# Optimization experiments

Hardware: AMD Instinct MI355X
Metric: run time of the kernel (lower is better)

The kernel has to match this reference:

```python
import jax, jax.numpy as jnp
import numpy as np

N, NFEAT, NHID, NCLASS, HEADS, NLAYERS, E = 10000, 128, 64, 16, 4, 4, 160000
DT = 0.01
EPS = 1e-05


def _rmsnorm(x):
    rms = jnp.sqrt(jnp.mean(x * x, axis=-1, keepdims=True) + EPS)
    return x / rms


def setup_inputs() -> dict:
    key = jax.random.key(0)
    ks = jax.random.split(key, 16)
    s = lambda fi, fo: 1.0 / np.sqrt(fi)
    def lin(k, fi, fo):
        k1, k2 = jax.random.split(k)
        lim = 1.0 / np.sqrt(fi)
        return (jax.random.uniform(k1, (fi, fo), jnp.float32, -lim, lim),
                jax.random.uniform(k2, (fo,), jnp.float32, -lim, lim))
    x = jax.random.normal(ks[0], (N, NFEAT), jnp.float32)
    edge_index = jax.random.randint(ks[1], (2, E), 0, N, dtype=jnp.int64)
    enc_w, enc_b = lin(ks[2], NFEAT, NHID)
    dec_w, dec_b = lin(ks[3], NHID, NCLASS)
    lo_w, lo_b = lin(ks[4], NHID * HEADS, NHID)
    dpl_w, dpl_b = lin(ks[5], NHID, NHID * HEADS)
    dpr_w, dpr_b = lin(ks[6], NHID, NHID * HEADS)
    lin_w, lin_b = lin(ks[7], NHID, NHID * HEADS)
    att = jax.random.normal(ks[8], (HEADS, NHID), jnp.float32) * (1.0 / np.sqrt(NHID))
    return dict(x=x, enc_w=enc_w, enc_b=enc_b, dec_w=dec_w, dec_b=dec_b,
                lo_w=lo_w, lo_b=lo_b, dpl_w=dpl_w, dpl_b=dpl_b,
                dpr_w=dpr_w, dpr_b=dpr_b, lin_w=lin_w, lin_b=lin_b,
                att=att, edge_index=edge_index)


def reference(x, enc_w, enc_b, dec_w, dec_b, lo_w, lo_b, dpl_w, dpl_b,
              dpr_w, dpr_b, lin_w, lin_b, att, edge_index):
    row, col = edge_index[0], edge_index[1]  # src, dst

    # dynamics constants (learnable_dyn_params=False)
    omega = jax.nn.softplus(jnp.float32(1.0))
    zeta = jax.nn.softplus(jnp.float32(1.0))
    Ks = jax.nn.softplus(jnp.float32(1.0))
    omega_sq = omega * omega

    Y = jax.nn.relu(x @ enc_w + enc_b)              # [N, nhid]
    X = Y

    # fixed GATv2 attention projections from Y_0
    xl = (Y @ dpl_w + dpl_b).reshape(N, HEADS, NHID)  # [N,H,C]
    xr = (Y @ dpr_w + dpr_b).reshape(N, HEADS, NHID)

    # symmetric GCN normalization on edges
    deg = jax.ops.segment_sum(jnp.ones((E,), jnp.float32), col, num_segments=N)
    dis = jnp.where(deg > 0, deg ** -0.5, 0.0)
    norm = dis[row] * dis[col]                       # [E]

    # edge attention logits are fixed across layers (depend only on Y_0)
    e_feat = jax.nn.leaky_relu(xl[row] + xr[col], 0.2)      # [E,H,C]
    score = jnp.einsum('ehc,hc->eh', e_feat, att)           # [E,H]
    smax = jax.ops.segment_max(score, col, num_segments=N)  # [N,H]
    a = jnp.exp(score - smax[col])
    ssum = jax.ops.segment_sum(a, col, num_segments=N)      # [N,H]
    alpha = a / jnp.where(ssum[col] > 0, ssum[col], 1.0)    # [E,H]
    w_edge = alpha * norm[:, None]                          # [E,H]

    for _ in range(NLAYERS):
        v = (Y @ lin_w + lin_b).reshape(N, HEADS, NHID)     # value projection
        msg = v[row] * w_edge[:, :, None]                   # [E,H,C]
        coupling = jax.ops.segment_sum(msg, col, num_segments=N).reshape(N, HEADS * NHID)
        coupling_Y = coupling @ lo_w + lo_b                 # [N, nhid]
        Y = Y + DT * (-2.0 * zeta * omega * Y - omega_sq * X + Ks * coupling_Y)
        X = X + DT * Y
        X = _rmsnorm(X)
        Y = _rmsnorm(Y)

    return X @ dec_w + dec_b                                # [N, nclass]
```

## Files before the change

### kernel.cpp

```cpp
#include <hip/hip_runtime.h>
#include <math.h>

#define NFEAT 128
#define HC    256
#define NCLS  16
#define DT_F  0.01f
#define EPS_F 1e-5f

__device__ __forceinline__ unsigned char f2f8(float f) {
  int v = __builtin_amdgcn_cvt_pk_fp8_f32(f, f, 0, false);
  return (unsigned char)(v & 0xff);
}
__device__ __forceinline__ float f82f(unsigned int b) {
  return __builtin_amdgcn_cvt_f32_fp8((int)b, 0);
}
__device__ __forceinline__ float f82f_sel0(unsigned int w) { return __builtin_amdgcn_cvt_f32_fp8((int)w, 0); }
__device__ __forceinline__ float f82f_sel1(unsigned int w) { return __builtin_amdgcn_cvt_f32_fp8((int)w, 1); }
__device__ __forceinline__ float f82f_sel2(unsigned int w) { return __builtin_amdgcn_cvt_f32_fp8((int)w, 2); }
__device__ __forceinline__ float f82f_sel3(unsigned int w) { return __builtin_amdgcn_cvt_f32_fp8((int)w, 3); }

__device__ __forceinline__ float edge_logit(unsigned int w, float4 r4, float4 at4) {
  float vx = f82f_sel0(w) + r4.x, vy = f82f_sel1(w) + r4.y;
  float vz = f82f_sel2(w) + r4.z, vw = f82f_sel3(w) + r4.w;
  vx = fmaxf(vx, 0.2f * vx); vy = fmaxf(vy, 0.2f * vy);
  vz = fmaxf(vz, 0.2f * vz); vw = fmaxf(vw, 0.2f * vw);
  float t = vx * at4.x;
  t = fmaf(vy, at4.y, t); t = fmaf(vz, at4.z, t); t = fmaf(vw, at4.w, t);
  return t;
}

__global__ __launch_bounds__(256) void enc_kernel(
    const float* __restrict__ x, const float* __restrict__ w,
    const float* __restrict__ b, float* __restrict__ Y, float* __restrict__ X,
    unsigned char* __restrict__ Ybf, int* __restrict__ deg, int n) {
  __shared__ float ws[NFEAT * 64];
  const int gtid = blockIdx.x * 256 + threadIdx.x, GSZ = gridDim.x * 256;
  for (int t = gtid; t < n; t += GSZ) deg[t] = 0;
  for (int t = threadIdx.x; t < NFEAT * 64; t += blockDim.x) ws[t] = w[t];
  __syncthreads();
  const int wave = threadIdx.x >> 6, lane = threadIdx.x & 63;
  for (int i = blockIdx.x * 4 + wave; i < n; i += gridDim.x * 4) {
    const float* xr = x + (size_t)i * NFEAT;
    float acc = b[lane];
#pragma unroll 8
    for (int k = 0; k < NFEAT; ++k) acc = fmaf(xr[k], ws[k * 64 + lane], acc);
    acc = fmaxf(acc, 0.f);
    const size_t idx = (size_t)i * 64 + lane;
    Y[idx] = acc; X[idx] = acc; Ybf[idx] = f2f8(acc);
  }
}

__global__ __launch_bounds__(256) void proj_kernel(
    const float* __restrict__ Y,
    const float* __restrict__ wl, const float* __restrict__ bl,
    const float* __restrict__ wr, const float* __restrict__ br,
    const int* __restrict__ col, const float* __restrict__ lin_w,
    const float* __restrict__ lin_b, const float* __restrict__ lo_w,
    unsigned char* __restrict__ xlb, float* __restrict__ xr,
    float* __restrict__ Wext, float* __restrict__ bb, int* __restrict__ deg,
    int n, int E) {
  const int half = gridDim.x >> 1;
  const bool doR = (int)blockIdx.x < half;
  const int bid = doR ? blockIdx.x : blockIdx.x - half;
  const float* __restrict__ W = doR ? wr : wl;
  const float* __restrict__ B = doR ? br : bl;
  float wreg[64];
  const int t = threadIdx.x;
#pragma unroll
  for (int k = 0; k < 64; ++k) wreg[k] = W[k * HC + t];
  const float bias = B[t];
  for (int i0 = bid * 4; i0 < n; i0 += half * 4) {
    const float* ap = Y + (size_t)i0 * 64;
    float a0 = bias, a1 = bias, a2 = bias, a3 = bias;
#pragma unroll
    for (int k = 0; k < 64; ++k) {
      const float w = wreg[k];
      a0 = fmaf(ap[k], w, a0);
      a1 = fmaf(ap[64 + k], w, a1);
      a2 = fmaf(ap[128 + k], w, a2);
      a3 = fmaf(ap[192 + k], w, a3);
    }
    if (doR) {
      if (i0 + 0 < n) xr[(size_t)(i0 + 0) * HC + t] = a0;
      if (i0 + 1 < n) xr[(size_t)(i0 + 1) * HC + t] = a1;
      if (i0 + 2 < n) xr[(size_t)(i0 + 2) * HC + t] = a2;
      if (i0 + 3 < n) xr[(size_t)(i0 + 3) * HC + t] = a3;
    } else {
      if (i0 + 0 < n) xlb[(size_t)(i0 + 0) * HC + t] = f2f8(a0);
      if (i0 + 1 < n) xlb[(size_t)(i0 + 1) * HC + t] = f2f8(a1);
      if (i0 + 2 < n) xlb[(size_t)(i0 + 2) * HC + t] = f2f8(a2);
      if (i0 + 3 < n) xlb[(size_t)(i0 + 3) * HC + t] = f2f8(a3);
    }
  }
  const int gtid = blockIdx.x * 256 + t, GSZ = gridDim.x * 256;
  for (int e = gtid; e < E; e += GSZ) atomicAdd(&deg[col[e]], 1);
  for (int f = gtid; f < 260 * 64; f += GSZ) {
    const int b2 = f >> 6, j = f & 63;
    float a = 0.f;
    if (b2 < 256) {
      const int k = b2 >> 2, h = b2 & 3;
#pragma unroll 8
      for (int c = 0; c < 64; ++c)
        a = fmaf(lin_w[k * HC + h * 64 + c], lo_w[(size_t)(h * 64 + c) * 64 + j], a);
      Wext[b2 * 64 + j] = a;
    } else {
      const int h = b2 - 256;
#pragma unroll 8
      for (int c = 0; c < 64; ++c)
        a = fmaf(lin_b[h * 64 + c], lo_w[(size_t)(h * 64 + c) * 64 + j], a);
      bb[h * 64 + j] = a;
    }
  }
}

__global__ __launch_bounds__(1024) void scan_kernel(
    const int* __restrict__ deg, int* __restrict__ offsets, int* __restrict__ cursor,
    float* __restrict__ dis, int n) {
  __shared__ int part[1024];
  const int t = threadIdx.x;
  const int chunk = (n + 1023) / 1024;
  const int start = t * chunk;
  const int end = min(start + chunk, n);
  int s = 0;
  for (int i = start; i < end; ++i) s += deg[i];
  part[t] = s;
  __syncthreads();
  for (int off = 1; off < 1024; off <<= 1) {
    int v = (t >= off) ? part[t - off] : 0;
    __syncthreads();
    part[t] += v;
    __syncthreads();
  }
  int run = (t == 0) ? 0 : part[t - 1];
  for (int i = start; i < end; ++i) {
    offsets[i] = run;
    cursor[i] = run;
    const int d = deg[i];
    dis[i] = (d > 0) ? rsqrtf((float)d) : 0.f;
    run += d;
  }
}

__global__ __launch_bounds__(256) void scatter_kernel(
    const int* __restrict__ row, const int* __restrict__ col,
    int* __restrict__ cursor, int* __restrict__ srow, int E) {
  int e = blockIdx.x * blockDim.x + threadIdx.x;
  if (e >= E) return;
  int pos = atomicAdd(&cursor[col[e]], 1);
  srow[pos] = row[e];
}

__global__ __launch_bounds__(256, 8) void score_layer1(
    const int* __restrict__ offs, const int* __restrict__ deg,
    const int* __restrict__ srow,
    const unsigned char* __restrict__ xlb, const float* __restrict__ xr,
    const float* __restrict__ att, const float* __restrict__ dis,
    const float* __restrict__ bb, const float* __restrict__ lo_b,
    const float* __restrict__ Wext, const unsigned char* __restrict__ ybf_in,
    const float* __restrict__ Yin, float* __restrict__ Yout,
    unsigned char* __restrict__ ybf_out, float* __restrict__ X,
    float4* __restrict__ sw, float4* __restrict__ invq, float* __restrict__ fb,
    int n, float c_decay, float c_x, float c_k) {
  const int tid = threadIdx.x, wave = tid >> 6, lane = tid & 63;
  __shared__ float aggl[4][HC];
  __shared__ float partl[4][4][64];
  const float4 at4 = ((const float4*)att)[lane];
  const unsigned int* xlb4 = (const unsigned int*)xlb;
  const float4* xr4 = (const float4*)xr;
  const int i = blockIdx.x * 4 + wave;
  float g0 = 0.f, g1 = 0.f, g2 = 0.f, g3 = 0.f;
  float fbv = 0.f;
  if (i < n) {
    const int s = offs[i], e = s + deg[i];
    if (s >= e) {
      if (lane == 0) invq[i] = make_float4(0.f, 0.f, 0.f, 0.f);
      fbv = lo_b[lane];
      fb[(size_t)i * 64 + lane] = fbv;
    } else {
      const float4 r4 = xr4[(size_t)i * 64 + lane];
      const float dd = dis[i];
      float ssum = 0.f, wsum = 0.f;
      int p = s;
      int n0 = 0, n1 = 0, n2 = 0, n3 = 0;
      if (p + 3 < e) { n0 = srow[p]; n1 = srow[p + 1]; n2 = srow[p + 2]; n3 = srow[p + 3]; }
      while (p + 3 < e) {
        const int q0 = n0, q1 = n1, q2 = n2, q3 = n3;
        const int pn = p + 4;
        if (pn + 3 < e) { n0 = srow[pn]; n1 = srow[pn + 1]; n2 = srow[pn + 2]; n3 = srow[pn + 3]; }
        const unsigned int u0 = xlb4[(size_t)q0 * 64 + lane];
        const unsigned int u1 = xlb4[(size_t)q1 * 64 + lane];
        const unsigned int u2 = xlb4[(size_t)q2 * 64 + lane];
        const unsigned int u3 = xlb4[(size_t)q3 * 64 + lane];
        const float di0 = dis[q0], di1 = dis[q1], di2 = dis[q2], di3 = dis[q3];
        const float ya = f82f(ybf_in[(size_t)q0 * 64 + lane]);
        const float yb = f82f(ybf_in[(size_t)q1 * 64 + lane]);
        const float yc = f82f(ybf_in[(size_t)q2 * 64 + lane]);
        const float yd = f82f(ybf_in[(size_t)q3 * 64 + lane]);
        float t0 = edge_logit(u0, r4, at4);
        float t1 = edge_logit(u1, r4, at4);
        float t2 = edge_logit(u2, r4, at4);
        float t3 = edge_logit(u3, r4, at4);
#pragma unroll
        for (int m = 1; m < 16; m <<= 1) {
          t0 += __shfl_xor(t0, m);
          t1 += __shfl_xor(t1, m);
          t2 += __shfl_xor(t2, m);
          t3 += __shfl_xor(t3, m);
        }
        const float a0 = __expf(t0), a1 = __expf(t1), a2 = __expf(t2), a3 = __expf(t3);
        ssum += (a0 + a1) + (a2 + a3);
        const float sv0 = a0 * di0, sv1 = a1 * di1, sv2 = a2 * di2, sv3 = a3 * di3;
        wsum += (sv0 + sv1) + (sv2 + sv3);
        if ((lane & 15) == 0) {
          ((float*)&sw[p])[lane >> 4] = sv0;
          ((float*)&sw[p + 1])[lane >> 4] = sv1;
          ((float*)&sw[p + 2])[lane >> 4] = sv2;
          ((float*)&sw[p + 3])[lane >> 4] = sv3;
        }
        const float sa0 = __shfl(sv0, 0), sa1 = __shfl(sv0, 16);
        const float sa2 = __shfl(sv0, 32), sa3 = __shfl(sv0, 48);
        g0 = fmaf(sa0, ya, g0); g1 = fmaf(sa1, ya, g1);
        g2 = fmaf(sa2, ya, g2); g3 = fmaf(sa3, ya, g3);
        const float sb0 = __shfl(sv1, 0), sb1 = __shfl(sv1, 16);
        const float sb2 = __shfl(sv1, 32), sb3 = __shfl(sv1, 48);
        g0 = fmaf(sb0, yb, g0); g1 = fmaf(sb1, yb, g1);
        g2 = fmaf(sb2, yb, g2); g3 = fmaf(sb3, yb, g3);
        const float sc0 = __shfl(sv2, 0), sc1 = __shfl(sv2, 16);
        const float sc2 = __shfl(sv2, 32), sc3 = __shfl(sv2, 48);
        g0 = fmaf(sc0, yc, g0); g1 = fmaf(sc1, yc, g1);
        g2 = fmaf(sc2, yc, g2); g3 = fmaf(sc3, yc, g3);
        const float sd0 = __shfl(sv3, 0), sd1 = __shfl(sv3, 16);
        const float sd2 = __shfl(sv3, 32), sd3 = __shfl(sv3, 48);
        g0 = fmaf(sd0, yd, g0); g1 = fmaf(sd1, yd, g1);
        g2 = fmaf(sd2, yd, g2); g3 = fmaf(sd3, yd, g3);
        p = pn;
      }
      for (; p < e; ++p) {
        const int ra = srow[p];
        const unsigned int u0 = xlb4[(size_t)ra * 64 + lane];
        const float dia = dis[ra];
        const float ya = f82f(ybf_in[(size_t)ra * 64 + lane]);
        float t0 = edge_logit(u0, r4, at4);
#pragma unroll
        for (int m = 1; m < 16; m <<= 1) t0 += __shfl_xor(t0, m);
        const float a0 = __expf(t0);
        ssum += a0;
        const float sv0 = a0 * dia;
        wsum += sv0;
        if ((lane & 15) == 0) ((float*)&sw[p])[lane >> 4] = sv0;
        const float sa0 = __shfl(sv0, 0), sa1 = __shfl(sv0, 16);
        const float sa2 = __shfl(sv0, 32), sa3 = __shfl(sv0, 48);
        g0 = fmaf(sa0, ya, g0); g1 = fmaf(sa1, ya, g1);
        g2 = fmaf(sa2, ya, g2); g3 = fmaf(sa3, ya, g3);
      }
      const float inv = dd / (ssum > 0.f ? ssum : 1.f);
      if ((lane & 15) == 0) ((float*)&invq[i])[lane >> 4] = inv;
      const float i0h = __shfl(inv, 0), i1h = __shfl(inv, 16);
      const float i2h = __shfl(inv, 32), i3h = __shfl(inv, 48);
      g0 *= i0h; g1 *= i1h; g2 *= i2h; g3 *= i3h;
      const float wqv = wsum * inv;
      const float w0 = __shfl(wqv, 0), w1 = __shfl(wqv, 16);
      const float w2 = __shfl(wqv, 32), w3 = __shfl(wqv, 48);
      fbv = lo_b[lane];
      fbv = fmaf(w0, bb[lane], fbv);
      fbv = fmaf(w1, bb[64 + lane], fbv);
      fbv = fmaf(w2, bb[128 + lane], fbv);
      fbv = fmaf(w3, bb[192 + lane], fbv);
      fb[(size_t)i * 64 + lane] = fbv;
    }
  }
  float4 o; o.x = g0; o.y = g1; o.z = g2; o.w = g3;
  ((float4*)aggl[wave])[lane] = o;
  __syncthreads();
  float p0 = 0.f, p1 = 0.f, p2 = 0.f, p3 = 0.f;
  const float* __restrict__ wrow = Wext + (wave * 64) * 64 + lane;
#pragma unroll
  for (int q4 = 0; q4 < 16; ++q4) {
    const float4 b0 = *(const float4*)(&aggl[0][wave * 64 + q4 * 4]);
    const float4 b1 = *(const float4*)(&aggl[1][wave * 64 + q4 * 4]);
    const float4 b2 = *(const float4*)(&aggl[2][wave * 64 + q4 * 4]);
    const float4 b3 = *(const float4*)(&aggl[3][wave * 64 + q4 * 4]);
    const float w0 = wrow[(q4 * 4 + 0) * 64];
    const float w1 = wrow[(q4 * 4 + 1) * 64];
    const float w2 = wrow[(q4 * 4 + 2) * 64];
    const float w3 = wrow[(q4 * 4 + 3) * 64];
    p0 = fmaf(b0.x, w0, p0); p0 = fmaf(b0.y, w1, p0);
    p0 = fmaf(b0.z, w2, p0); p0 = fmaf(b0.w, w3, p0);
    p1 = fmaf(b1.x, w0, p1); p1 = fmaf(b1.y, w1, p1);
    p1 = fmaf(b1.z, w2, p1); p1 = fmaf(b1.w, w3, p1);
    p2 = fmaf(b2.x, w0, p2); p2 = fmaf(b2.y, w1, p2);
    p2 = fmaf(b2.z, w2, p2); p2 = fmaf(b2.w, w3, p2);
    p3 = fmaf(b3.x, w0, p3); p3 = fmaf(b3.y, w1, p3);
    p3 = fmaf(b3.z, w2, p3); p3 = fmaf(b3.w, w3, p3);
  }
  partl[wave][0][lane] = p0;
  partl[wave][1][lane] = p1;
  partl[wave][2][lane] = p2;
  partl[wave][3][lane] = p3;
  __syncthreads();
  if (i < n) {
    const size_t idx = (size_t)i * 64 + lane;
    float outv = fbv;
    outv += partl[0][wave][lane] + partl[1][wave][lane] +
            partl[2][wave][lane] + partl[3][wave][lane];
    const float y = Yin[idx], xv = X[idx];
    const float yn = fmaf(c_k, outv, fmaf(c_x, xv, c_decay * y));
    const float xn = fmaf(DT_F, yn, xv);
    float sy = yn * yn, sx = xn * xn;
#pragma unroll
    for (int m = 32; m > 0; m >>= 1) {
      sy += __shfl_xor(sy, m);
      sx += __shfl_xor(sx, m);
    }
    const float ynn = yn * rsqrtf(sy * (1.f / 64.f) + EPS_F);
    Yout[idx] = ynn;
    ybf_out[idx] = f2f8(ynn);
    X[idx] = xn * rsqrtf(sx * (1.f / 64.f) + EPS_F);
  }
}

__global__ __launch_bounds__(256, 8) void layer_fused(
    const int* __restrict__ offs, const int* __restrict__ deg,
    const int* __restrict__ srow,
    const float4* __restrict__ sw, const float4* __restrict__ invq,
    const unsigned char* __restrict__ ybf_in, const float* __restrict__ Wext,
    const float* __restrict__ fb, const float* __restrict__ Yin,
    float* __restrict__ Yout, unsigned char* __restrict__ ybf_out,
    float* __restrict__ X, int n, float c_decay, float c_x, float c_k) {
  const int t = threadIdx.x, tr = t >> 6, lane = t & 63;
  __shared__ float aggl[4][HC];
  __shared__ float partl[4][4][64];
  const int i = blockIdx.x * 4 + tr;
  float4 o = make_float4(0.f, 0.f, 0.f, 0.f);
  if (i < n) {
    const int s = offs[i], e = s + deg[i];
    float a0 = 0.f, a1 = 0.f, a2 = 0.f, a3 = 0.f;
    int p = s;
    int n0 = 0, n1 = 0, n2 = 0, n3 = 0;
    if (p + 3 < e) { n0 = srow[p]; n1 = srow[p + 1]; n2 = srow[p + 2]; n3 = srow[p + 3]; }
    while (p + 3 < e) {
      const int q0 = n0, q1 = n1, q2 = n2, q3 = n3;
      const int pn = p + 4;
      if (pn + 3 < e) { n0 = srow[pn]; n1 = srow[pn + 1]; n2 = srow[pn + 2]; n3 = srow[pn + 3]; }
      const float4 v0 = sw[p], v1 = sw[p + 1], v2 = sw[p + 2], v3 = sw[p + 3];
      const float y0 = f82f(ybf_in[(size_t)q0 * 64 + lane]);
      const float y1 = f82f(ybf_in[(size_t)q1 * 64 + lane]);
      const float y2 = f82f(ybf_in[(size_t)q2 * 64 + lane]);
      const float y3 = f82f(ybf_in[(size_t)q3 * 64 + lane]);
      a0 = fmaf(v0.x, y0, a0); a1 = fmaf(v0.y, y0, a1);
      a2 = fmaf(v0.z, y0, a2); a3 = fmaf(v0.w, y0, a3);
      a0 = fmaf(v1.x, y1, a0); a1 = fmaf(v1.y, y1, a1);
      a2 = fmaf(v1.z, y1, a2); a3 = fmaf(v1.w, y1, a3);
      a0 = fmaf(v2.x, y2, a0); a1 = fmaf(v2.y, y2, a1);
      a2 = fmaf(v2.z, y2, a2); a3 = fmaf(v2.w, y2, a3);
      a0 = fmaf(v3.x, y3, a0); a1 = fmaf(v3.y, y3, a1);
      a2 = fmaf(v3.z, y3, a2); a3 = fmaf(v3.w, y3, a3);
      p = pn;
    }
    for (; p < e; ++p) {
      const int r0 = srow[p];
      const float4 v0 = sw[p];
      const float y0 = f82f(ybf_in[(size_t)r0 * 64 + lane]);
      a0 = fmaf(v0.x, y0, a0); a1 = fmaf(v0.y, y0, a1);
      a2 = fmaf(v0.z, y0, a2); a3 = fmaf(v0.w, y0, a3);
    }
    const float4 iv = invq[i];
    o.x = a0 * iv.x; o.y = a1 * iv.y; o.z = a2 * iv.z; o.w = a3 * iv.w;
  }
  ((float4*)aggl[tr])[lane] = o;
  __syncthreads();
  float p0 = 0.f, p1 = 0.f, p2 = 0.f, p3 = 0.f;
  const float* __restrict__ wrow = Wext + (tr * 64) * 64 + lane;
#pragma unroll
  for (int q4 = 0; q4 < 16; ++q4) {
    const float4 b0 = *(const float4*)(&aggl[0][tr * 64 + q4 * 4]);
    const float4 b1 = *(const float4*)(&aggl[1][tr * 64 + q4 * 4]);
    const float4 b2 = *(const float4*)(&aggl[2][tr * 64 + q4 * 4]);
    const float4 b3 = *(const float4*)(&aggl[3][tr * 64 + q4 * 4]);
    const float w0 = wrow[(q4 * 4 + 0) * 64];
    const float w1 = wrow[(q4 * 4 + 1) * 64];
    const float w2 = wrow[(q4 * 4 + 2) * 64];
    const float w3 = wrow[(q4 * 4 + 3) * 64];
    p0 = fmaf(b0.x, w0, p0); p0 = fmaf(b0.y, w1, p0);
    p0 = fmaf(b0.z, w2, p0); p0 = fmaf(b0.w, w3, p0);
    p1 = fmaf(b1.x, w0, p1); p1 = fmaf(b1.y, w1, p1);
    p1 = fmaf(b1.z, w2, p1); p1 = fmaf(b1.w, w3, p1);
    p2 = fmaf(b2.x, w0, p2); p2 = fmaf(b2.y, w1, p2);
    p2 = fmaf(b2.z, w2, p2); p2 = fmaf(b2.w, w3, p2);
    p3 = fmaf(b3.x, w0, p3); p3 = fmaf(b3.y, w1, p3);
    p3 = fmaf(b3.z, w2, p3); p3 = fmaf(b3.w, w3, p3);
  }
  partl[tr][0][lane] = p0;
  partl[tr][1][lane] = p1;
  partl[tr][2][lane] = p2;
  partl[tr][3][lane] = p3;
  __syncthreads();
  if (i < n) {
    const size_t idx = (size_t)i * 64 + lane;
    float outv = fb[idx];
    outv += partl[0][tr][lane] + partl[1][tr][lane] +
            partl[2][tr][lane] + partl[3][tr][lane];
    const float y = Yin[idx], xv = X[idx];
    const float yn = fmaf(c_k, outv, fmaf(c_x, xv, c_decay * y));
    const float xn = fmaf(DT_F, yn, xv);
    float sy = yn * yn, sx = xn * xn;
#pragma unroll
    for (int m = 32; m > 0; m >>= 1) {
      sy += __shfl_xor(sy, m);
      sx += __shfl_xor(sx, m);
    }
    const float ynn = yn * rsqrtf(sy * (1.f / 64.f) + EPS_F);
    Yout[idx] = ynn;
    ybf_out[idx] = f2f8(ynn);
    X[idx] = xn * rsqrtf(sx * (1.f / 64.f) + EPS_F);
  }
}

__global__ __launch_bounds__(256, 8) void layer_last_dec(
    const int* __restrict__ offs, const int* __restrict__ deg,
    const int* __restrict__ srow,
    const float4* __restrict__ sw, const float4* __restrict__ invq,
    const unsigned char* __restrict__ ybf_in, const float* __restrict__ Wext,
    const float* __restrict__ fb, const float* __restrict__ Yin,
    const float* __restrict__ X,
    const float* __restrict__ dec_w, const float* __restrict__ dec_b,
    float* __restrict__ out, int n, float c_decay, float c_x, float c_k) {
  const int t = threadIdx.x, tr = t >> 6, lane = t & 63;
  __shared__ float aggl[4][HC];
  __shared__ float partl[4][4][64];
  const int i = blockIdx.x * 4 + tr;
  float4 o = make_float4(0.f, 0.f, 0.f, 0.f);
  if (i < n) {
    const int s = offs[i], e = s + deg[i];
    float a0 = 0.f, a1 = 0.f, a2 = 0.f, a3 = 0.f;
    int p = s;
    int n0 = 0, n1 = 0, n2 = 0, n3 = 0;
    if (p + 3 < e) { n0 = srow[p]; n1 = srow[p + 1]; n2 = srow[p + 2]; n3 = srow[p + 3]; }
    while (p + 3 < e) {
      const int q0 = n0, q1 = n1, q2 = n2, q3 = n3;
      const int pn = p + 4;
      if (pn + 3 < e) { n0 = srow[pn]; n1 = srow[pn + 1]; n2 = srow[pn + 2]; n3 = srow[pn + 3]; }
      const float4 v0 = sw[p], v1 = sw[p + 1], v2 = sw[p + 2], v3 = sw[p + 3];
      const float y0 = f82f(ybf_in[(size_t)q0 * 64 + lane]);
      const float y1 = f82f(ybf_in[(size_t)q1 * 64 + lane]);
      const float y2 = f82f(ybf_in[(size_t)q2 * 64 + lane]);
      const float y3 = f82f(ybf_in[(size_t)q3 * 64 + lane]);
      a0 = fmaf(v0.x, y0, a0); a1 = fmaf(v0.y, y0, a1);
      a2 = fmaf(v0.z, y0, a2); a3 = fmaf(v0.w, y0, a3);
      a0 = fmaf(v1.x, y1, a0); a1 = fmaf(v1.y, y1, a1);
      a2 = fmaf(v1.z, y1, a2); a3 = fmaf(v1.w, y1, a3);
      a0 = fmaf(v2.x, y2, a0); a1 = fmaf(v2.y, y2, a1);
      a2 = fmaf(v2.z, y2, a2); a3 = fmaf(v2.w, y2, a3);
      a0 = fmaf(v3.x, y3, a0); a1 = fmaf(v3.y, y3, a1);
      a2 = fmaf(v3.z, y3, a2); a3 = fmaf(v3.w, y3, a3);
      p = pn;
    }
    for (; p < e; ++p) {
      const int r0 = srow[p];
      const float4 v0 = sw[p];
      const float y0 = f82f(ybf_in[(size_t)r0 * 64 + lane]);
      a0 = fmaf(v0.x, y0, a0); a1 = fmaf(v0.y, y0, a1);
      a2 = fmaf(v0.z, y0, a2); a3 = fmaf(v0.w, y0, a3);
    }
    const float4 iv = invq[i];
    o.x = a0 * iv.x; o.y = a1 * iv.y; o.z = a2 * iv.z; o.w = a3 * iv.w;
  }
  ((float4*)aggl[tr])[lane] = o;
  __syncthreads();
  float p0 = 0.f, p1 = 0.f, p2 = 0.f, p3 = 0.f;
  const float* __restrict__ wrow = Wext + (tr * 64) * 64 + lane;
#pragma unroll
  for (int q4 = 0; q4 < 16; ++q4) {
    const float4 b0 = *(const float4*)(&aggl[0][tr * 64 + q4 * 4]);
    const float4 b1 = *(const float4*)(&aggl[1][tr * 64 + q4 * 4]);
    const float4 b2 = *(const float4*)(&aggl[2][tr * 64 + q4 * 4]);
    const float4 b3 = *(const float4*)(&aggl[3][tr * 64 + q4 * 4]);
    const float w0 = wrow[(q4 * 4 + 0) * 64];
    const float w1 = wrow[(q4 * 4 + 1) * 64];
    const float w2 = wrow[(q4 * 4 + 2) * 64];
    const float w3 = wrow[(q4 * 4 + 3) * 64];
    p0 = fmaf(b0.x, w0, p0); p0 = fmaf(b0.y, w1, p0);
    p0 = fmaf(b0.z, w2, p0); p0 = fmaf(b0.w, w3, p0);
    p1 = fmaf(b1.x, w0, p1); p1 = fmaf(b1.y, w1, p1);
    p1 = fmaf(b1.z, w2, p1); p1 = fmaf(b1.w, w3, p1);
    p2 = fmaf(b2.x, w0, p2); p2 = fmaf(b2.y, w1, p2);
    p2 = fmaf(b2.z, w2, p2); p2 = fmaf(b2.w, w3, p2);
    p3 = fmaf(b3.x, w0, p3); p3 = fmaf(b3.y, w1, p3);
    p3 = fmaf(b3.z, w2, p3); p3 = fmaf(b3.w, w3, p3);
  }
  partl[tr][0][lane] = p0;
  partl[tr][1][lane] = p1;
  partl[tr][2][lane] = p2;
  partl[tr][3][lane] = p3;
  __syncthreads();
  if (i < n) {
    const size_t idx = (size_t)i * 64 + lane;
    float outv = fb[idx];
    outv += partl[0][tr][lane] + partl[1][tr][lane] +
            partl[2][tr][lane] + partl[3][tr][lane];
    const float y = Yin[idx], xv = X[idx];
    const float yn = fmaf(c_k, outv, fmaf(c_x, xv, c_decay * y));
    const float xn = fmaf(DT_F, yn, xv);
    float sx = xn * xn;
#pragma unroll
    for (int m = 32; m > 0; m >>= 1) sx += __shfl_xor(sx, m);
    const float xnn = xn * rsqrtf(sx * (1.f / 64.f) + EPS_F);
    aggl[tr][lane] = xnn;
    const int j = lane & 15, kq = lane >> 4;
    float a = 0.f;
#pragma unroll
    for (int k2 = 0; k2 < 16; ++k2) {
      const int k = kq * 16 + k2;
      a = fmaf(aggl[tr][k], dec_w[k * NCLS + j], a);
    }
    a += __shfl_xor(a, 16);
    a += __shfl_xor(a, 32);
    if (lane < 16) out[(size_t)i * NCLS + lane] = a + dec_b[lane];
  }
}

static inline size_t alignup(size_t x) { return (x + 255) & ~(size_t)255; }

extern "C" void kernel_launch(void* const* d_in, const int* in_sizes, int n_in,
                              void* d_out, int out_size, void* d_ws, size_t ws_size,
                              hipStream_t stream) {
  const float* x     = (const float*)d_in[0];
  const float* enc_w = (const float*)d_in[1];
  const float* enc_b = (const float*)d_in[2];
  const float* dec_w = (const float*)d_in[3];
  const float* dec_b = (const float*)d_in[4];
  const float* lo_w  = (const float*)d_in[5];
  const float* lo_b  = (const float*)d_in[6];
  const float* dpl_w = (const float*)d_in[7];
  const float* dpl_b = (const float*)d_in[8];
  const float* dpr_w = (const float*)d_in[9];
  const float* dpr_b = (const float*)d_in[10];
  const float* lin_w = (const float*)d_in[11];
  const float* lin_b = (const float*)d_in[12];
  const float* att   = (const float*)d_in[13];
  const int*   ei    = (const int*)d_in[14];

  const int n = in_sizes[0] / NFEAT;
  const int E = in_sizes[14] / 2;
  const int* row = ei;
  const int* col = ei + E;

  char* p = (char*)d_ws;
  size_t off = 0;
  auto alloc = [&](size_t bytes) { void* r = p + off; off += alignup(bytes); return r; };
  float*         Y    = (float*)alloc((size_t)n * 64 * 4);
  float*         Y2   = (float*)alloc((size_t)n * 64 * 4);
  float*         X    = (float*)alloc((size_t)n * 64 * 4);
  unsigned char* ybfA = (unsigned char*)alloc((size_t)n * 64);
  unsigned char* ybfB = (unsigned char*)alloc((size_t)n * 64);
  unsigned char* xlb  = (unsigned char*)alloc((size_t)n * HC);
  float*         xr   = (float*)alloc((size_t)n * HC * 4);
  float4*        sw   = (float4*)alloc((size_t)E * 16);
  int*           srow = (int*)alloc((size_t)E * 4);
  int*           deg  = (int*)alloc((size_t)n * 4);
  int*           offs = (int*)alloc((size_t)(n + 1) * 4);
  int*           cur  = (int*)alloc((size_t)n * 4);
  float*         dis  = (float*)alloc((size_t)n * 4);
  float4*        invq = (float4*)alloc((size_t)n * 16);
  float*         fb   = (float*)alloc((size_t)n * 64 * 4);
  float*         Wext = (float*)alloc((size_t)HC * 64 * 4);
  float*         bb   = (float*)alloc((size_t)HC * 4);

  const double sp = log1p(exp(1.0));
  const float c_decay = (float)(1.0 - 2.0 * sp * sp * 0.01);
  const float c_x     = (float)(-(sp * sp) * 0.01);
  const float c_k     = (float)(sp * 0.01);

  const int quads = (n + 3) / 4;

  enc_kernel<<<512, 256, 0, stream>>>(x, enc_w, enc_b, Y, X, ybfA, deg, n);
  proj_kernel<<<1024, 256, 0, stream>>>(Y, dpl_w, dpl_b, dpr_w, dpr_b, col,
                                        lin_w, lin_b, lo_w, xlb, xr, Wext, bb, deg,
                                        n, E);
  scan_kernel<<<1, 1024, 0, stream>>>(deg, offs, cur, dis, n);
  scatter_kernel<<<(E + 255) / 256, 256, 0, stream>>>(row, col, cur, srow, E);
  score_layer1<<<quads, 256, 0, stream>>>(offs, deg, srow, xlb, xr, att, dis, bb, lo_b,
                                          Wext, ybfA, Y, Y2, ybfB, X, sw, invq, fb,
                                          n, c_decay, c_x, c_k);
  layer_fused<<<quads, 256, 0, stream>>>(offs, deg, srow, sw, invq, ybfB, Wext, fb,
                                         Y2, Y, ybfA, X, n, c_decay, c_x, c_k);
  layer_fused<<<quads, 256, 0, stream>>>(offs, deg, srow, sw, invq, ybfA, Wext, fb,
                                         Y, Y2, ybfB, X, n, c_decay, c_x, c_k);
  layer_last_dec<<<quads, 256, 0, stream>>>(offs, deg, srow, sw, invq, ybfB, Wext, fb,
                                            Y2, X, dec_w, dec_b, (float*)d_out,
                                            n, c_decay, c_x, c_k);
}
```

Before: 176.3 us.

## Pack edge source index and fp8 attention weights into one int2 record

The per-edge float4 weights and the separate source-index array are replaced by one 8-byte record per edge: the source index plus four per-head weights quantized to fp8. The later layer kernels then read a single record per edge instead of an int and a float4, which cuts edge-metadata traffic. The edge loops also drop their scalar remainder loop and use a masked, padded 4-wide loop. In exchange the attention weights lose precision through fp8 quantization, and each edge does a few extra convert instructions.

```diff
diff --git a/kernel.cpp b/kernel.cpp
--- a/kernel.cpp
+++ b/kernel.cpp
@@ -18,6 +18,10 @@
 __device__ __forceinline__ float f82f_sel1(unsigned int w) { return __builtin_amdgcn_cvt_f32_fp8((int)w, 1); }
 __device__ __forceinline__ float f82f_sel2(unsigned int w) { return __builtin_amdgcn_cvt_f32_fp8((int)w, 2); }
 __device__ __forceinline__ float f82f_sel3(unsigned int w) { return __builtin_amdgcn_cvt_f32_fp8((int)w, 3); }
+__device__ __forceinline__ unsigned int pk4f8(float a, float b, float c, float d) {
+  int lo = __builtin_amdgcn_cvt_pk_fp8_f32(a, b, 0, false);
+  return (unsigned int)__builtin_amdgcn_cvt_pk_fp8_f32(c, d, lo, true);
+}
 
 __device__ __forceinline__ float edge_logit(unsigned int w, float4 r4, float4 at4) {
   float vx = f82f_sel0(w) + r4.x, vy = f82f_sel1(w) + r4.y;
@@ -159,7 +163,7 @@
     const float* __restrict__ Wext, const unsigned char* __restrict__ ybf_in,
     const float* __restrict__ Yin, float* __restrict__ Yout,
     unsigned char* __restrict__ ybf_out, float* __restrict__ X,
-    float4* __restrict__ sw, float4* __restrict__ invq, float* __restrict__ fb,
+    int2* __restrict__ erec, float4* __restrict__ invq, float* __restrict__ fb,
     int n, float c_decay, float c_x, float c_k) {
   const int tid = threadIdx.x, wave = tid >> 6, lane = tid & 63;
   __shared__ float aggl[4][HC];
@@ -180,13 +184,19 @@
       const float4 r4 = xr4[(size_t)i * 64 + lane];
       const float dd = dis[i];
       float ssum = 0.f, wsum = 0.f;
-      int p = s;
-      int n0 = 0, n1 = 0, n2 = 0, n3 = 0;
-      if (p + 3 < e) { n0 = srow[p]; n1 = srow[p + 1]; n2 = srow[p + 2]; n3 = srow[p + 3]; }
-      while (p + 3 < e) {
-        const int q0 = n0, q1 = n1, q2 = n2, q3 = n3;
+      int id0 = srow[s];
+      int id1 = srow[(s + 1 < e) ? s + 1 : e - 1];
+      int id2 = srow[(s + 2 < e) ? s + 2 : e - 1];
+      int id3 = srow[(s + 3 < e) ? s + 3 : e - 1];
+      for (int p = s; p < e; p += 4) {
+        const int q0 = id0, q1 = id1, q2 = id2, q3 = id3;
         const int pn = p + 4;
-        if (pn + 3 < e) { n0 = srow[pn]; n1 = srow[pn + 1]; n2 = srow[pn + 2]; n3 = srow[pn + 3]; }
+        if (pn < e) {
+          id0 = srow[pn];
+          id1 = srow[(pn + 1 < e) ? pn + 1 : e - 1];
+          id2 = srow[(pn + 2 < e) ? pn + 2 : e - 1];
+          id3 = srow[(pn + 3 < e) ? pn + 3 : e - 1];
+        }
         const unsigned int u0 = xlb4[(size_t)q0 * 64 + lane];
         const unsigned int u1 = xlb4[(size_t)q1 * 64 + lane];
         const unsigned int u2 = xlb4[(size_t)q2 * 64 + lane];
@@ -207,16 +217,16 @@
           t2 += __shfl_xor(t2, m);
           t3 += __shfl_xor(t3, m);
         }
-        const float a0 = __expf(t0), a1 = __expf(t1), a2 = __expf(t2), a3 = __expf(t3);
+        const float m1 = (p + 1 < e) ? 1.f : 0.f;
+        const float m2 = (p + 2 < e) ? 1.f : 0.f;
+        const float m3 = (p + 3 < e) ? 1.f : 0.f;
+        const float a0 = __expf(t0);
+        const float a1 = __expf(t1) * m1;
+        const float a2 = __expf(t2) * m2;
+        const float a3 = __expf(t3) * m3;
         ssum += (a0 + a1) + (a2 + a3);
         const float sv0 = a0 * di0, sv1 = a1 * di1, sv2 = a2 * di2, sv3 = a3 * di3;
         wsum += (sv0 + sv1) + (sv2 + sv3);
-        if ((lane & 15) == 0) {
-          ((float*)&sw[p])[lane >> 4] = sv0;
-          ((float*)&sw[p + 1])[lane >> 4] = sv1;
-          ((float*)&sw[p + 2])[lane >> 4] = sv2;
-          ((float*)&sw[p + 3])[lane >> 4] = sv3;
-        }
         const float sa0 = __shfl(sv0, 0), sa1 = __shfl(sv0, 16);
         const float sa2 = __shfl(sv0, 32), sa3 = __shfl(sv0, 48);
         g0 = fmaf(sa0, ya, g0); g1 = fmaf(sa1, ya, g1);
@@ -233,25 +243,12 @@
         const float sd2 = __shfl(sv3, 32), sd3 = __shfl(sv3, 48);
         g0 = fmaf(sd0, yd, g0); g1 = fmaf(sd1, yd, g1);
         g2 = fmaf(sd2, yd, g2); g3 = fmaf(sd3, yd, g3);
-        p = pn;
-      }
-      for (; p < e; ++p) {
-        const int ra = srow[p];
-        const unsigned int u0 = xlb4[(size_t)ra * 64 + lane];
-        const float dia = dis[ra];
-        const float ya = f82f(ybf_in[(size_t)ra * 64 + lane]);
-        float t0 = edge_logit(u0, r4, at4);
-#pragma unroll
-        for (int m = 1; m < 16; m <<= 1) t0 += __shfl_xor(t0, m);
-        const float a0 = __expf(t0);
-        ssum += a0;
-        const float sv0 = a0 * dia;
-        wsum += sv0;
-        if ((lane & 15) == 0) ((float*)&sw[p])[lane >> 4] = sv0;
-        const float sa0 = __shfl(sv0, 0), sa1 = __shfl(sv0, 16);
-        const float sa2 = __shfl(sv0, 32), sa3 = __shfl(sv0, 48);
-        g0 = fmaf(sa0, ya, g0); g1 = fmaf(sa1, ya, g1);
-        g2 = fmaf(sa2, ya, g2); g3 = fmaf(sa3, ya, g3);
+        if (lane == 0) {
+          erec[p] = make_int2(q0, (int)pk4f8(sa0, sa1, sa2, sa3));
+          if (p + 1 < e) erec[p + 1] = make_int2(q1, (int)pk4f8(sb0, sb1, sb2, sb3));
+          if (p + 2 < e) erec[p + 2] = make_int2(q2, (int)pk4f8(sc0, sc1, sc2, sc3));
+          if (p + 3 < e) erec[p + 3] = make_int2(q3, (int)pk4f8(sd0, sd1, sd2, sd3));
+        }
       }
       const float inv = dd / (ssum > 0.f ? ssum : 1.f);
       if ((lane & 15) == 0) ((float*)&invq[i])[lane >> 4] = inv;
@@ -321,8 +318,7 @@
 
 __global__ __launch_bounds__(256, 8) void layer_fused(
     const int* __restrict__ offs, const int* __restrict__ deg,
-    const int* __restrict__ srow,
-    const float4* __restrict__ sw, const float4* __restrict__ invq,
+    const int2* __restrict__ erec, const float4* __restrict__ invq,
     const unsigned char* __restrict__ ybf_in, const float* __restrict__ Wext,
     const float* __restrict__ fb, const float* __restrict__ Yin,
     float* __restrict__ Yout, unsigned char* __restrict__ ybf_out,
@@ -334,38 +330,42 @@
   float4 o = make_float4(0.f, 0.f, 0.f, 0.f);
   if (i < n) {
     const int s = offs[i], e = s + deg[i];
-    float a0 = 0.f, a1 = 0.f, a2 = 0.f, a3 = 0.f;
-    int p = s;
-    int n0 = 0, n1 = 0, n2 = 0, n3 = 0;
-    if (p + 3 < e) { n0 = srow[p]; n1 = srow[p + 1]; n2 = srow[p + 2]; n3 = srow[p + 3]; }
-    while (p + 3 < e) {
-      const int q0 = n0, q1 = n1, q2 = n2, q3 = n3;
-      const int pn = p + 4;
-      if (pn + 3 < e) { n0 = srow[pn]; n1 = srow[pn + 1]; n2 = srow[pn + 2]; n3 = srow[pn + 3]; }
-      const float4 v0 = sw[p], v1 = sw[p + 1], v2 = sw[p + 2], v3 = sw[p + 3];
-      const float y0 = f82f(ybf_in[(size_t)q0 * 64 + lane]);
-      const float y1 = f82f(ybf_in[(size_t)q1 * 64 + lane]);
-      const float y2 = f82f(ybf_in[(size_t)q2 * 64 + lane]);
-      const float y3 = f82f(ybf_in[(size_t)q3 * 64 + lane]);
-      a0 = fmaf(v0.x, y0, a0); a1 = fmaf(v0.y, y0, a1);
-      a2 = fmaf(v0.z, y0, a2); a3 = fmaf(v0.w, y0, a3);
-      a0 = fmaf(v1.x, y1, a0); a1 = fmaf(v1.y, y1, a1);
-      a2 = fmaf(v1.z, y1, a2); a3 = fmaf(v1.w, y1, a3);
-      a0 = fmaf(v2.x, y2, a0); a1 = fmaf(v2.y, y2, a1);
-      a2 = fmaf(v2.z, y2, a2); a3 = fmaf(v2.w, y2, a3);
-      a0 = fmaf(v3.x, y3, a0); a1 = fmaf(v3.y, y3, a1);
-      a2 = fmaf(v3.z, y3, a2); a3 = fmaf(v3.w, y3, a3);
-      p = pn;
-    }
-    for (; p < e; ++p) {
-      const int r0 = srow[p];
-      const float4 v0 = sw[p];
-      const float y0 = f82f(ybf_in[(size_t)r0 * 64 + lane]);
-      a0 = fmaf(v0.x, y0, a0); a1 = fmaf(v0.y, y0, a1);
-      a2 = fmaf(v0.z, y0, a2); a3 = fmaf(v0.w, y0, a3);
-    }
-    const float4 iv = invq[i];
-    o.x = a0 * iv.x; o.y = a1 * iv.y; o.z = a2 * iv.z; o.w = a3 * iv.w;
+    if (s < e) {
+      float a0 = 0.f, a1 = 0.f, a2 = 0.f, a3 = 0.f;
+      int2 r0 = erec[s];
+      int2 r1 = erec[(s + 1 < e) ? s + 1 : e - 1];
+      int2 r2 = erec[(s + 2 < e) ? s + 2 : e - 1];
+      int2 r3 = erec[(s + 3 < e) ? s + 3 : e - 1];
+      for (int p = s; p < e; p += 4) {
+        const int2 c0 = r0, c1 = r1, c2 = r2, c3 = r3;
+        const int pn = p + 4;
+        if (pn < e) {
+          r0 = erec[pn];
+          r1 = erec[(pn + 1 < e) ? pn + 1 : e - 1];
+          r2 = erec[(pn + 2 < e) ? pn + 2 : e - 1];
+          r3 = erec[(pn + 3 < e) ? pn + 3 : e - 1];
+        }
+        const float m1 = (p + 1 < e) ? 1.f : 0.f;
+        const float m2 = (p + 2 < e) ? 1.f : 0.f;
+        const float m3 = (p + 3 < e) ? 1.f : 0.f;
+        const float y0 = f82f(ybf_in[(size_t)c0.x * 64 + lane]);
+        const float y1 = f82f(ybf_in[(size_t)c1.x * 64 + lane]) * m1;
+        const float y2 = f82f(ybf_in[(size_t)c2.x * 64 + lane]) * m2;
+        const float y3 = f82f(ybf_in[(size_t)c3.x * 64 + lane]) * m3;
+        const unsigned int w0 = (unsigned int)c0.y, w1 = (unsigned int)c1.y;
+        const unsigned int w2 = (unsigned int)c2.y, w3 = (unsigned int)c3.y;
+        a0 = fmaf(f82f_sel0(w0), y0, a0); a1 = fmaf(f82f_sel1(w0), y0, a1);
+        a2 = fmaf(f82f_sel2(w0), y0, a2); a3 = fmaf(f82f_sel3(w0), y0, a3);
+        a0 = fmaf(f82f_sel0(w1), y1, a0); a1 = fmaf(f82f_sel1(w1), y1, a1);
+        a2 = fmaf(f82f_sel2(w1), y1, a2); a3 = fmaf(f82f_sel3(w1), y1, a3);
+        a0 = fmaf(f82f_sel0(w2), y2, a0); a1 = fmaf(f82f_sel1(w2), y2, a1);
+        a2 = fmaf(f82f_sel2(w2), y2, a2); a3 = fmaf(f82f_sel3(w2), y2, a3);
+        a0 = fmaf(f82f_sel0(w3), y3, a0); a1 = fmaf(f82f_sel1(w3), y3, a1);
+        a2 = fmaf(f82f_sel2(w3), y3, a2); a3 = fmaf(f82f_sel3(w3), y3, a3);
+      }
+      const float4 iv = invq[i];
+      o.x = a0 * iv.x; o.y = a1 * iv.y; o.z = a2 * iv.z; o.w = a3 * iv.w;
+    }
   }
   ((float4*)aggl[tr])[lane] = o;
   __syncthreads();
@@ -418,8 +418,7 @@
 
 __global__ __launch_bounds__(256, 8) void layer_last_dec(
     const int* __restrict__ offs, const int* __restrict__ deg,
-    const int* __restrict__ srow,
-    const float4* __restrict__ sw, const float4* __restrict__ invq,
+    const int2* __restrict__ erec, const float4* __restrict__ invq,
     const unsigned char* __restrict__ ybf_in, const float* __restrict__ Wext,
     const float* __restrict__ fb, const float* __restrict__ Yin,
     const float* __restrict__ X,
@@ -432,38 +431,42 @@
   float4 o = make_float4(0.f, 0.f, 0.f, 0.f);
   if (i < n) {
     const int s = offs[i], e = s + deg[i];
-    float a0 = 0.f, a1 = 0.f, a2 = 0.f, a3 = 0.f;
-    int p = s;
-    int n0 = 0, n1 = 0, n2 = 0, n3 = 0;
-    if (p + 3 < e) { n0 = srow[p]; n1 = srow[p + 1]; n2 = srow[p + 2]; n3 = srow[p + 3]; }
-    while (p + 3 < e) {
-      const int q0 = n0, q1 = n1, q2 = n2, q3 = n3;
-      const int pn = p + 4;
-      if (pn + 3 < e) { n0 = srow[pn]; n1 = srow[pn + 1]; n2 = srow[pn + 2]; n3 = srow[pn + 3]; }
-      const float4 v0 = sw[p], v1 = sw[p + 1], v2 = sw[p + 2], v3 = sw[p + 3];
-      const float y0 = f82f(ybf_in[(size_t)q0 * 64 + lane]);
-      const float y1 = f82f(ybf_in[(size_t)q1 * 64 + lane]);
-      const float y2 = f82f(ybf_in[(size_t)q2 * 64 + lane]);
-      const float y3 = f82f(ybf_in[(size_t)q3 * 64 + lane]);
-      a0 = fmaf(v0.x, y0, a0); a1 = fmaf(v0.y, y0, a1);
-      a2 = fmaf(v0.z, y0, a2); a3 = fmaf(v0.w, y0, a3);
-      a0 = fmaf(v1.x, y1, a0); a1 = fmaf(v1.y, y1, a1);
-      a2 = fmaf(v1.z, y1, a2); a3 = fmaf(v1.w, y1, a3);
-      a0 = fmaf(v2.x, y2, a0); a1 = fmaf(v2.y, y2, a1);
-      a2 = fmaf(v2.z, y2, a2); a3 = fmaf(v2.w, y2, a3);
-      a0 = fmaf(v3.x, y3, a0); a1 = fmaf(v3.y, y3, a1);
-      a2 = fmaf(v3.z, y3, a2); a3 = fmaf(v3.w, y3, a3);
-      p = pn;
-    }
-    for (; p < e; ++p) {
-      const int r0 = srow[p];
-      const float4 v0 = sw[p];
-      const float y0 = f82f(ybf_in[(size_t)r0 * 64 + lane]);
-      a0 = fmaf(v0.x, y0, a0); a1 = fmaf(v0.y, y0, a1);
-      a2 = fmaf(v0.z, y0, a2); a3 = fmaf(v0.w, y0, a3);
-    }
-    const float4 iv = invq[i];
-    o.x = a0 * iv.x; o.y = a1 * iv.y; o.z = a2 * iv.z; o.w = a3 * iv.w;
+    if (s < e) {
+      float a0 = 0.f, a1 = 0.f, a2 = 0.f, a3 = 0.f;
+      int2 r0 = erec[s];
+      int2 r1 = erec[(s + 1 < e) ? s + 1 : e - 1];
+      int2 r2 = erec[(s + 2 < e) ? s + 2 : e - 1];
+      int2 r3 = erec[(s + 3 < e) ? s + 3 : e - 1];
+      for (int p = s; p < e; p += 4) {
+        const int2 c0 = r0, c1 = r1, c2 = r2, c3 = r3;
+        const int pn = p + 4;
+        if (pn < e) {
+          r0 = erec[pn];
+          r1 = erec[(pn + 1 < e) ? pn + 1 : e - 1];
+          r2 = erec[(pn + 2 < e) ? pn + 2 : e - 1];
+          r3 = erec[(pn + 3 < e) ? pn + 3 : e - 1];
+        }
+        const float m1 = (p + 1 < e) ? 1.f : 0.f;
+        const float m2 = (p + 2 < e) ? 1.f : 0.f;
+        const float m3 = (p + 3 < e) ? 1.f : 0.f;
+        const float y0 = f82f(ybf_in[(size_t)c0.x * 64 + lane]);
+        const float y1 = f82f(ybf_in[(size_t)c1.x * 64 + lane]) * m1;
+        const float y2 = f82f(ybf_in[(size_t)c2.x * 64 + lane]) * m2;
+        const float y3 = f82f(ybf_in[(size_t)c3.x * 64 + lane]) * m3;
+        const unsigned int w0 = (unsigned int)c0.y, w1 = (unsigned int)c1.y;
+        const unsigned int w2 = (unsigned int)c2.y, w3 = (unsigned int)c3.y;
+        a0 = fmaf(f82f_sel0(w0), y0, a0); a1 = fmaf(f82f_sel1(w0), y0, a1);
+        a2 = fmaf(f82f_sel2(w0), y0, a2); a3 = fmaf(f82f_sel3(w0), y0, a3);
+        a0 = fmaf(f82f_sel0(w1), y1, a0); a1 = fmaf(f82f_sel1(w1), y1, a1);
+        a2 = fmaf(f82f_sel2(w1), y1, a2); a3 = fmaf(f82f_sel3(w1), y1, a3);
+        a0 = fmaf(f82f_sel0(w2), y2, a0); a1 = fmaf(f82f_sel1(w2), y2, a1);
+        a2 = fmaf(f82f_sel2(w2), y2, a2); a3 = fmaf(f82f_sel3(w2), y2, a3);
+        a0 = fmaf(f82f_sel0(w3), y3, a0); a1 = fmaf(f82f_sel1(w3), y3, a1);
+        a2 = fmaf(f82f_sel2(w3), y3, a2); a3 = fmaf(f82f_sel3(w3), y3, a3);
+      }
+      const float4 iv = invq[i];
+      o.x = a0 * iv.x; o.y = a1 * iv.y; o.z = a2 * iv.z; o.w = a3 * iv.w;
+    }
   }
   ((float4*)aggl[tr])[lane] = o;
   __syncthreads();
@@ -555,7 +558,7 @@
   unsigned char* ybfB = (unsigned char*)alloc((size_t)n * 64);
   unsigned char* xlb  = (unsigned char*)alloc((size_t)n * HC);
   float*         xr   = (float*)alloc((size_t)n * HC * 4);
-  float4*        sw   = (float4*)alloc((size_t)E * 16);
+  int2*          erec = (int2*)alloc((size_t)E * 8);
   int*           srow = (int*)alloc((size_t)E * 4);
   int*           deg  = (int*)alloc((size_t)n * 4);
   int*           offs = (int*)alloc((size_t)(n + 1) * 4);
@@ -580,13 +583,13 @@
   scan_kernel<<<1, 1024, 0, stream>>>(deg, offs, cur, dis, n);
   scatter_kernel<<<(E + 255) / 256, 256, 0, stream>>>(row, col, cur, srow, E);
   score_layer1<<<quads, 256, 0, stream>>>(offs, deg, srow, xlb, xr, att, dis, bb, lo_b,
-                                          Wext, ybfA, Y, Y2, ybfB, X, sw, invq, fb,
+                                          Wext, ybfA, Y, Y2, ybfB, X, erec, invq, fb,
                                           n, c_decay, c_x, c_k);
-  layer_fused<<<quads, 256, 0, stream>>>(offs, deg, srow, sw, invq, ybfB, Wext, fb,
+  layer_fused<<<quads, 256, 0, stream>>>(offs, deg, erec, invq, ybfB, Wext, fb,
                                          Y2, Y, ybfA, X, n, c_decay, c_x, c_k);
-  layer_fused<<<quads, 256, 0, stream>>>(offs, deg, srow, sw, invq, ybfA, Wext, fb,
+  layer_fused<<<quads, 256, 0, stream>>>(offs, deg, erec, invq, ybfA, Wext, fb,
                                          Y, Y2, ybfB, X, n, c_decay, c_x, c_k);
-  layer_last_dec<<<quads, 256, 0, stream>>>(offs, deg, srow, sw, invq, ybfB, Wext, fb,
+  layer_last_dec<<<quads, 256, 0, stream>>>(offs, deg, erec, invq, ybfB, Wext, fb,
                                             Y2, X, dec_w, dec_b, (float*)d_out,
                                             n, c_decay, c_x, c_k);
 }
```

New measurement: 177.4 us. About the same (+0.6%).
